# Kernel tuning notes

Hardware: AMD Instinct MI355X
Metric: run time of the kernel (lower is better)

Reference implementation:

```python
import jax, jax.numpy as jnp
import numpy as np

PAD = 3  # 7x7 conv, padding=3 (same as nn.Conv2d(257, 1, 7, padding=3))


def setup_inputs() -> dict:
    key = jax.random.key(0)
    k1, k2, k3 = jax.random.split(key, 3)
    N, C, H, W, T = 2, 256, 16, 16, 8
    feat = jax.random.normal(k1, (N, C, H, W), dtype=jnp.float32)
    # mask_init_conv weight/bias: Conv2d(in=C+1, out=1, k=7)
    w = jax.random.normal(k2, (1, C + 1, 7, 7), dtype=jnp.float32) * 0.02
    b = jnp.zeros((1,), dtype=jnp.float32)
    # binary instance masks at level 7: [N, T, H, W]
    targets = jax.random.randint(k3, (N, T, H, W), 0, 2).astype(jnp.int32)
    return {"feat": feat, "w": w, "b": b, "targets": targets}


def reference(feat, w, b, targets):
    N, C, H, W = feat.shape
    P = H * W
    T = targets.shape[1]

    # --- init_inst_pyramid, batched over all H*W positions ---
    # each position gets the shared feature plus its own one-hot plane
    onehot = jnp.eye(P, dtype=feat.dtype).reshape(P, 1, H, W)          # [P,1,H,W]
    x = jnp.concatenate(
        [jnp.broadcast_to(feat[:, None], (N, P, C, H, W)),
         jnp.broadcast_to(onehot[None], (N, P, 1, H, W))], axis=2
    ).reshape(N * P, C + 1, H, W)
    masks = jax.lax.conv_general_dilated(
        x, w, window_strides=(1, 1), padding=[(PAD, PAD), (PAD, PAD)],
        dimension_numbers=("NCHW", "OIHW", "NCHW"))
    masks = masks.reshape(N, P, H, W) + b[0]                           # [N,P,H,W]
    m = jax.nn.sigmoid(masks)

    # --- loss_of_pyramid_7, vectorized over positions ---
    tf = targets.astype(feat.dtype)                                    # [N,T,H,W]
    areas = tf.sum(axis=(2, 3))                                        # [N,T]
    on = tf.reshape(N, T, P).transpose(0, 2, 1)                        # [N,P,T]
    cnt = on.sum(-1)                                                   # [N,P]
    # among instances active at this position, pick the smallest-area one
    masked_area = jnp.where(on > 0, areas[:, None, :], jnp.inf)        # [N,P,T]
    idx = jnp.argmin(masked_area, axis=-1)                             # [N,P]
    chosen = tf[jnp.arange(N)[:, None], idx]                           # [N,P,H,W]

    loss_pos = jnp.abs(m - chosen).mean(axis=(-2, -1))                 # [N,P]
    sum_t = tf.sum(axis=1)                                             # [N,H,W]
    loss_neg = (sum_t[:, None] * m).mean(axis=(-2, -1))                # [N,P]
    loss = jnp.where(cnt > 0, loss_pos, loss_neg).sum()
    return loss
```

## Files before the change

### kernel.cpp

```cpp
#include <hip/hip_runtime.h>
#include <math.h>

#define N_    2
#define C_    256
#define H_    16
#define W_    16
#define T_    8
#define P_    256
#define PAD_  3
#define CPC_  4
#define CHUNKS_ (C_ / CPC_)
#define NB_BASE_ (N_ * CHUNKS_)
#define ROWS_ 24
#define PLSZ_ (ROWS_ * ROWS_)


__global__ void k1_conv(const float* __restrict__ feat,
                        const float* __restrict__ wt,
                        float* __restrict__ ws,
                        float* __restrict__ out) {
    int b = blockIdx.x;
    int tid = threadIdx.x;
    __shared__ float pl[CPC_ * PLSZ_];
    __shared__ float wsm[CPC_ * 49];

    int n = b / CHUNKS_;
    int chunk = b % CHUNKS_;
    int c0 = chunk * CPC_;

    float4* z4 = (float4*)pl;
    #pragma unroll
    for (int i = tid; i < CPC_ * PLSZ_ / 4; i += 256)
        z4[i] = make_float4(0.f, 0.f, 0.f, 0.f);
    if (tid < CPC_ * 49) wsm[tid] = wt[c0 * 49 + tid];
    __syncthreads();

    {
        const float4* src4 = (const float4*)(feat + (size_t)(n * C_ + c0) * P_);
        int c  = tid >> 6;
        int r  = tid & 63;
        int hh = r >> 2;
        int w4 = r & 3;
        *(float4*)(pl + c * PLSZ_ + (hh + 3) * ROWS_ + 4 + w4 * 4) = src4[tid];
    }
    __syncthreads();

    int h = tid >> 4, w = tid & 15;
    float acc[CPC_];
    #pragma unroll
    for (int c = 0; c < CPC_; ++c) acc[c] = 0.f;

    #pragma unroll
    for (int c = 0; c < CPC_; ++c) {
        const float* p  = pl + c * PLSZ_ + h * ROWS_ + (w + 1);
        const float* wc = wsm + c * 49;
        #pragma unroll
        for (int kh = 0; kh < 7; ++kh)
            #pragma unroll
            for (int kw = 0; kw < 7; ++kw)
                acc[c] += p[kh * ROWS_ + kw] * wc[kh * 7 + kw];
    }
    ws[(size_t)b * P_ + tid] = (acc[0] + acc[1]) + (acc[2] + acc[3]);

    if (b == 0 && tid == 0) out[0] = 0.f;
}

__global__ __launch_bounds__(1024)
void k2_loss(const float* __restrict__ wt,
             const float* __restrict__ bias,
             const int* __restrict__ tgt,
             const float* __restrict__ ws,
             float* __restrict__ out) {
    int b = blockIdx.x;
    int tid = threadIdx.x;
    int n = b >> 4, pg = b & 15;

    __shared__ float s_tgt[T_][P_];
    __shared__ float s_ktab[49];
    __shared__ float s_area[T_];
    __shared__ float s_st[P_];
    __shared__ int   s_cnt[16];
    __shared__ int   s_idx[16];
    __shared__ float s_red[16];

    for (int i = tid; i < T_ * P_; i += 1024)
        s_tgt[0][i] = (float)tgt[n * T_ * P_ + i];
    if (tid < 49) s_ktab[tid] = wt[C_ * 49 + tid];
    __syncthreads();

    int wave = tid >> 6, lane = tid & 63;
    if (wave < 8) {
        float v = s_tgt[wave][lane] + s_tgt[wave][lane + 64]
                + s_tgt[wave][lane + 128] + s_tgt[wave][lane + 192];
        #pragma unroll
        for (int off = 32; off; off >>= 1) v += __shfl_down(v, off, 64);
        if (lane == 0) s_area[wave] = v;
    } else if (wave < 12) {
        int pix = tid - 512;
        float s = 0.f;
        #pragma unroll
        for (int t = 0; t < T_; ++t) s += s_tgt[t][pix];
        s_st[pix] = s;
    }
    __syncthreads();

    if (tid < 16) {
        int p = pg * 16 + tid;
        int cnt = 0; float best = 3.402823466e38f; int idx = 0;
        #pragma unroll
        for (int t = 0; t < T_; ++t) {
            float on = s_tgt[t][p];
            cnt += (int)on;
            if (on > 0.f && s_area[t] < best) { best = s_area[t]; idx = t; }
        }
        s_cnt[tid] = cnt; s_idx[tid] = idx;
    }
    __syncthreads();

    int slot = tid >> 8;
    int pix  = tid & 255;
    int h = pix >> 4, wcol = pix & 15;

    float base = 0.f;
    const float* wsb = ws + (size_t)n * CHUNKS_ * P_ + pix;
    #pragma unroll
    for (int j = 0; j < CHUNKS_; ++j) base += wsb[j * P_];
    float bv = bias[0];
    float st = s_st[pix];

    float lsum = 0.f;
    #pragma unroll
    for (int it = 0; it < 4; ++it) {
        int pl_ = it * 4 + slot;
        int p = pg * 16 + pl_;
        int ph = p >> 4, pw = p & 15;
        int dh = ph - h + PAD_, dw = pw - wcol + PAD_;
        float kc = ((unsigned)dh < 7u && (unsigned)dw < 7u) ? s_ktab[dh * 7 + dw] : 0.f;
        float m = 1.f / (1.f + expf(-(base + kc + bv)));
        float contrib;
        if (s_cnt[pl_] > 0) contrib = fabsf(m - s_tgt[s_idx[pl_]][pix]);
        else                contrib = st * m;
        lsum += contrib;
    }

    #pragma unroll
    for (int off = 32; off; off >>= 1) lsum += __shfl_down(lsum, off, 64);
    if (lane == 0) s_red[wave] = lsum;
    __syncthreads();
    if (tid == 0) {
        float s = 0.f;
        #pragma unroll
        for (int i = 0; i < 16; ++i) s += s_red[i];
        atomicAdd(out, s * (1.0f / 256.0f));
    }
}

extern "C" void kernel_launch(void* const* d_in, const int* in_sizes, int n_in,
                              void* d_out, int out_size, void* d_ws, size_t ws_size,
                              hipStream_t stream) {
    const float* feat = (const float*)d_in[0];
    const float* wt   = (const float*)d_in[1];
    const float* bias = (const float*)d_in[2];
    const int*   tgt  = (const int*)d_in[3];
    float* out = (float*)d_out;
    float* ws  = (float*)d_ws;

    k1_conv<<<NB_BASE_, 256, 0, stream>>>(feat, wt, ws, out);
    k2_loss<<<N_ * 16, 1024, 0, stream>>>(wt, bias, tgt, ws, out);
}
```

Baseline: 16.16 us.

## Fuse conv and loss into one kernel with per-row-quad channel-parallel conv

Replaces the two-kernel pipeline (per-channel-chunk conv writing partials to workspace, then loss kernel summing them) with a single fused kernel. Each block handles one row and four output columns, loads a 7x12 halo patch for all 256 channels plus all weights into shared memory, computes one channel per thread and reduces across channels with shuffles, then computes the loss for all 256 positions at those four pixels. This removes the workspace round trip and one kernel launch, adding a memset launch instead. In exchange every block reloads the full weight tensor and about 100KB of shared memory, which limits occupancy.

```diff
diff --git a/kernel.cpp b/kernel.cpp
--- a/kernel.cpp
+++ b/kernel.cpp
@@ -1,111 +1,107 @@
 #include <hip/hip_runtime.h>
 #include <math.h>
 
-#define N_    2
-#define C_    256
-#define H_    16
-#define W_    16
-#define T_    8
-#define P_    256
-#define PAD_  3
-#define CPC_  4
-#define CHUNKS_ (C_ / CPC_)
-#define NB_BASE_ (N_ * CHUNKS_)
-#define ROWS_ 24
-#define PLSZ_ (ROWS_ * ROWS_)
+#define N_   2
+#define C_   256
+#define H_   16
+#define W_   16
+#define T_   8
+#define P_   256
+#define PW_  12
+#define PH_  7
+#define PSZ_ (PH_ * PW_)
 
 
-__global__ void k1_conv(const float* __restrict__ feat,
-                        const float* __restrict__ wt,
-                        float* __restrict__ ws,
-                        float* __restrict__ out) {
+__global__ __launch_bounds__(1024)
+void fused(const float* __restrict__ feat,
+           const float* __restrict__ wt,
+           const float* __restrict__ bias,
+           const int* __restrict__ tgt,
+           float* __restrict__ out) {
     int b = blockIdx.x;
     int tid = threadIdx.x;
-    __shared__ float pl[CPC_ * PLSZ_];
-    __shared__ float wsm[CPC_ * 49];
+    int n = b >> 6, h = (b >> 2) & 15, qx = b & 3;
 
-    int n = b / CHUNKS_;
-    int chunk = b % CHUNKS_;
-    int c0 = chunk * CPC_;
-
-    float4* z4 = (float4*)pl;
-    #pragma unroll
-    for (int i = tid; i < CPC_ * PLSZ_ / 4; i += 256)
-        z4[i] = make_float4(0.f, 0.f, 0.f, 0.f);
-    if (tid < CPC_ * 49) wsm[tid] = wt[c0 * 49 + tid];
-    __syncthreads();
+    __shared__ float pl[C_ * PSZ_];
+    __shared__ float wsm[C_ * 49];
+    __shared__ float s_tgt[T_][P_];
+    __shared__ float s_ktab[49];
+    __shared__ float s_area[T_];
+    __shared__ float s_st[4];
+    __shared__ int   s_cnt[P_];
+    __shared__ int   s_idx[P_];
+    __shared__ float s_base[4];
+    __shared__ float s_red[64];
 
     {
-        const float4* src4 = (const float4*)(feat + (size_t)(n * C_ + c0) * P_);
-        int c  = tid >> 6;
-        int r  = tid & 63;
-        int hh = r >> 2;
-        int w4 = r & 3;
-        *(float4*)(pl + c * PLSZ_ + (hh + 3) * ROWS_ + 4 + w4 * 4) = src4[tid];
+        const float4* f4 = (const float4*)(feat + (size_t)n * C_ * P_);
+        #pragma unroll
+        for (int k = 0; k < 6; ++k) {
+            int i = tid + k * 1024;
+            if (i < C_ * 21) {
+                int c  = i / 21, r = i - c * 21;
+                int kh = r / 3,  k4 = r - kh * 3;
+                int y   = h - 3 + kh;
+                int gc0 = qx * 4 - 4 + k4 * 4;
+                float4 v = make_float4(0.f, 0.f, 0.f, 0.f);
+                if ((unsigned)y < 16u && (unsigned)gc0 < 16u)
+                    v = f4[c * 64 + y * 4 + (gc0 >> 2)];
+                *(float4*)(pl + c * PSZ_ + kh * PW_ + k4 * 4) = v;
+            }
+        }
+        const float4* w4 = (const float4*)wt;
+        #pragma unroll
+        for (int k = 0; k < 4; ++k) {
+            int i = tid + k * 1024;
+            if (i < C_ * 49 / 4) ((float4*)wsm)[i] = w4[i];
+        }
+        for (int i = tid; i < T_ * P_; i += 1024)
+            s_tgt[0][i] = (float)tgt[n * T_ * P_ + i];
+        if (tid < 49) s_ktab[tid] = wt[C_ * 49 + tid];
     }
     __syncthreads();
 
-    int h = tid >> 4, w = tid & 15;
-    float acc[CPC_];
-    #pragma unroll
-    for (int c = 0; c < CPC_; ++c) acc[c] = 0.f;
+    int wid = tid >> 6, lane = tid & 63;
 
-    #pragma unroll
-    for (int c = 0; c < CPC_; ++c) {
-        const float* p  = pl + c * PLSZ_ + h * ROWS_ + (w + 1);
+    if (wid < T_) {
+        int t = wid;
+        float v = s_tgt[t][lane] + s_tgt[t][lane + 64]
+                + s_tgt[t][lane + 128] + s_tgt[t][lane + 192];
+        #pragma unroll
+        for (int off = 32; off; off >>= 1) v += __shfl_down(v, off, 64);
+        if (lane == 0) s_area[t] = v;
+    } else if (wid == 8 && lane < 4) {
+        int gpix = h * 16 + qx * 4 + lane;
+        float s = 0.f;
+        #pragma unroll
+        for (int t = 0; t < T_; ++t) s += s_tgt[t][gpix];
+        s_st[lane] = s;
+    }
+
+    int c  = tid >> 2;
+    int px = tid & 3;
+    float acc = 0.f;
+    {
+        const float* pp = pl + c * PSZ_ + (px + 1);
         const float* wc = wsm + c * 49;
         #pragma unroll
         for (int kh = 0; kh < 7; ++kh)
             #pragma unroll
             for (int kw = 0; kw < 7; ++kw)
-                acc[c] += p[kh * ROWS_ + kw] * wc[kh * 7 + kw];
+                acc += pp[kh * PW_ + kw] * wc[kh * 7 + kw];
     }
-    ws[(size_t)b * P_ + tid] = (acc[0] + acc[1]) + (acc[2] + acc[3]);
-
-    if (b == 0 && tid == 0) out[0] = 0.f;
-}
-
-__global__ __launch_bounds__(1024)
-void k2_loss(const float* __restrict__ wt,
-             const float* __restrict__ bias,
-             const int* __restrict__ tgt,
-             const float* __restrict__ ws,
-             float* __restrict__ out) {
-    int b = blockIdx.x;
-    int tid = threadIdx.x;
-    int n = b >> 4, pg = b & 15;
-
-    __shared__ float s_tgt[T_][P_];
-    __shared__ float s_ktab[49];
-    __shared__ float s_area[T_];
-    __shared__ float s_st[P_];
-    __shared__ int   s_cnt[16];
-    __shared__ int   s_idx[16];
-    __shared__ float s_red[16];
-
-    for (int i = tid; i < T_ * P_; i += 1024)
-        s_tgt[0][i] = (float)tgt[n * T_ * P_ + i];
-    if (tid < 49) s_ktab[tid] = wt[C_ * 49 + tid];
+    #pragma unroll
+    for (int off = 4; off < 64; off <<= 1) acc += __shfl_down(acc, off, 64);
+    if (lane < 4) s_red[wid * 4 + lane] = acc;
     __syncthreads();
 
-    int wave = tid >> 6, lane = tid & 63;
-    if (wave < 8) {
-        float v = s_tgt[wave][lane] + s_tgt[wave][lane + 64]
-                + s_tgt[wave][lane + 128] + s_tgt[wave][lane + 192];
-        #pragma unroll
-        for (int off = 32; off; off >>= 1) v += __shfl_down(v, off, 64);
-        if (lane == 0) s_area[wave] = v;
-    } else if (wave < 12) {
-        int pix = tid - 512;
+    if (tid < 4) {
         float s = 0.f;
         #pragma unroll
-        for (int t = 0; t < T_; ++t) s += s_tgt[t][pix];
-        s_st[pix] = s;
-    }
-    __syncthreads();
-
-    if (tid < 16) {
-        int p = pg * 16 + tid;
+        for (int wv = 0; wv < 16; ++wv) s += s_red[wv * 4 + tid];
+        s_base[tid] = s;
+    } else if (tid >= 64 && tid < 64 + P_) {
+        int p = tid - 64;
         int cnt = 0; float best = 3.402823466e38f; int idx = 0;
         #pragma unroll
         for (int t = 0; t < T_; ++t) {
@@ -113,39 +109,23 @@
             cnt += (int)on;
             if (on > 0.f && s_area[t] < best) { best = s_area[t]; idx = t; }
         }
-        s_cnt[tid] = cnt; s_idx[tid] = idx;
+        s_cnt[p] = cnt; s_idx[p] = idx;
     }
     __syncthreads();
 
-    int slot = tid >> 8;
-    int pix  = tid & 255;
-    int h = pix >> 4, wcol = pix & 15;
-
-    float base = 0.f;
-    const float* wsb = ws + (size_t)n * CHUNKS_ * P_ + pix;
-    #pragma unroll
-    for (int j = 0; j < CHUNKS_; ++j) base += wsb[j * P_];
     float bv = bias[0];
-    float st = s_st[pix];
-
-    float lsum = 0.f;
-    #pragma unroll
-    for (int it = 0; it < 4; ++it) {
-        int pl_ = it * 4 + slot;
-        int p = pg * 16 + pl_;
-        int ph = p >> 4, pw = p & 15;
-        int dh = ph - h + PAD_, dw = pw - wcol + PAD_;
-        float kc = ((unsigned)dh < 7u && (unsigned)dw < 7u) ? s_ktab[dh * 7 + dw] : 0.f;
-        float m = 1.f / (1.f + expf(-(base + kc + bv)));
-        float contrib;
-        if (s_cnt[pl_] > 0) contrib = fabsf(m - s_tgt[s_idx[pl_]][pix]);
-        else                contrib = st * m;
-        lsum += contrib;
-    }
+    int p = tid >> 2;
+    int gpix = h * 16 + qx * 4 + px;
+    int ph = p >> 4, pw = p & 15;
+    int dh = ph - h + 3, dw = pw - (qx * 4 + px) + 3;
+    float kc = ((unsigned)dh < 7u && (unsigned)dw < 7u) ? s_ktab[dh * 7 + dw] : 0.f;
+    float m = 1.f / (1.f + expf(-(s_base[px] + kc + bv)));
+    float contrib = (s_cnt[p] > 0) ? fabsf(m - s_tgt[s_idx[p]][gpix])
+                                   : s_st[px] * m;
 
     #pragma unroll
-    for (int off = 32; off; off >>= 1) lsum += __shfl_down(lsum, off, 64);
-    if (lane == 0) s_red[wave] = lsum;
+    for (int off = 32; off; off >>= 1) contrib += __shfl_down(contrib, off, 64);
+    if (lane == 0) s_red[wid] = contrib;
     __syncthreads();
     if (tid == 0) {
         float s = 0.f;
@@ -163,8 +143,7 @@
     const float* bias = (const float*)d_in[2];
     const int*   tgt  = (const int*)d_in[3];
     float* out = (float*)d_out;
-    float* ws  = (float*)d_ws;
 
-    k1_conv<<<NB_BASE_, 256, 0, stream>>>(feat, wt, ws, out);
-    k2_loss<<<N_ * 16, 1024, 0, stream>>>(wt, bias, tgt, ws, out);
+    hipMemsetAsync(out, 0, sizeof(float), stream);
+    fused<<<N_ * H_ * 4, 1024, 0, stream>>>(feat, wt, bias, tgt, out);
 }
```

After: 17.05 us. 1.06x slower.
